# Performance work log

Hardware: AMD Instinct MI355X
Metric: run time of the kernel (lower is better)

The kernel has to match this reference:

```python
import jax, jax.numpy as jnp
import numpy as np

N_QUBITS = 5
N_A = 1
Q_DEPTH = 6
PATCH = 2 ** (N_QUBITS - N_A)  # 16


def _cz_sign(w):
    # diagonal sign of CZ on wires (w, w+1) over a (2,)*N_QUBITS state grid
    s = np.ones((2,) * N_QUBITS, np.float32)
    idx = [slice(None)] * N_QUBITS
    idx[w] = 1
    idx[w + 1] = 1
    s[tuple(idx)] = -1.0
    return jnp.asarray(s)

CZ_SIGNS = [_cz_sign(w) for w in range(N_QUBITS - 1)]


def apply_ry(state, theta, wire):
    # state: (B, 2,2,2,2,2) real amplitudes; theta: scalar or (B,)
    c = jnp.cos(theta * 0.5)
    s = jnp.sin(theta * 0.5)
    if jnp.ndim(c) == 1:  # per-sample angle
        c = c[:, None, None, None, None]
        s = s[:, None, None, None, None]
    st = jnp.moveaxis(state, 1 + wire, -1)
    a0, a1 = st[..., 0], st[..., 1]
    out = jnp.stack([c * a0 - s * a1, s * a0 + c * a1], axis=-1)
    return jnp.moveaxis(out, -1, 1 + wire)


def run_generator(noise, weights):
    # noise: (B, 5) per-sample angles; weights: (6, 5) shared angles
    B = noise.shape[0]
    state = jnp.zeros((B,) + (2,) * N_QUBITS, noise.dtype)
    state = state.at[(slice(None),) + (0,) * N_QUBITS].set(1.0)  # |00000>
    for w in range(N_QUBITS):
        state = apply_ry(state, noise[:, w], w)
    for d in range(Q_DEPTH):
        for w in range(N_QUBITS):
            state = apply_ry(state, weights[d, w], w)
        for w in range(N_QUBITS - 1):
            state = state * CZ_SIGNS[w]
    # RY/CZ are real, so probs = amplitude^2; unitary => sum(probs)=1
    probs = state.reshape(B, 2 ** N_QUBITS) ** 2
    p0 = probs[:, :PATCH]
    p0 = p0 / jnp.sum(probs, axis=1, keepdims=True)
    return p0 / jnp.max(p0, axis=1, keepdims=True)


def setup_inputs() -> dict:
    key = jax.random.key(0)
    k1, k2 = jax.random.split(key)
    B, C, H, W = 262144, 1, 4, 4
    inp = jax.random.normal(k1, (B, C, H, W), dtype=jnp.float32)
    q_params = jax.random.uniform(k2, (4, Q_DEPTH * N_QUBITS), dtype=jnp.float32)  # q_delta=1
    return {"input": inp, "q_params": q_params}


def reference(input, q_params):
    B, C, H, W = input.shape
    k = 2  # scale_factor
    # bilinear (half-pixel / align_corners=False) upsample
    up = jax.image.resize(input, (B, C, H * k, W * k), method='linear')
    noise = up.reshape(B, -1)[:, :N_QUBITS]  # 5 angles per sample
    outs = [run_generator(noise, q_params[g].reshape(Q_DEPTH, N_QUBITS))
            for g in range(q_params.shape[0])]
    return jnp.concatenate(outs, axis=1)  # (B, n_generators * 16)
```

## Files before the change

### kernel.cpp

```cpp
#include <hip/hip_runtime.h>

#define NQ   5
#define QD   6
#define NGEN 4
#define NW   (NGEN * QD * NQ)

typedef float f32x4 __attribute__((ext_vector_type(4)));
typedef short short8 __attribute__((ext_vector_type(8)));

__device__ inline unsigned short f2bf_rne(float f) {
    unsigned u = __float_as_uint(f);
    u += 0x7FFFu + ((u >> 16) & 1u);
    return (unsigned short)(u >> 16);
}
__device__ inline float bf2f(unsigned short h) {
    return __uint_as_float(((unsigned)h) << 16);
}

__global__ __launch_bounds__(128) void qsrgan_build(
    const float* __restrict__ qp,
    unsigned short* __restrict__ Bh,
    unsigned short* __restrict__ Bl)
{
    __shared__ float cw[NW];
    __shared__ float sw[NW];
    const int t = threadIdx.x;
    if (t < NW) {
        float sv, cv;
        __sincosf(0.5f * qp[t], &sv, &cv);
        cw[t] = cv;
        sw[t] = sv;
    }
    __syncthreads();

    const int g = t >> 5;
    const int basis = t & 31;

    float st[32];
#pragma unroll
    for (int i = 0; i < 32; ++i) st[i] = (i == basis) ? 1.0f : 0.0f;

    for (int d = 0; d < QD; ++d) {
        const int base = g * (QD * NQ) + d * NQ;
#pragma unroll
        for (int w = 0; w < NQ; ++w) {
            const float cc = cw[base + w];
            const float ss = sw[base + w];
            const int stride = 1 << (4 - w);
#pragma unroll
            for (int i = 0; i < 32; ++i) {
                if (i & stride) continue;
                float a0 = st[i];
                float a1 = st[i + stride];
                st[i]          = cc * a0 - ss * a1;
                st[i + stride] = ss * a0 + cc * a1;
            }
        }
#pragma unroll
        for (int i = 0; i < 32; ++i) {
            int flips = 0;
#pragma unroll
            for (int w = 0; w < NQ - 1; ++w) {
                const int m = (1 << (4 - w)) | (1 << (3 - w));
                flips ^= ((i & m) == m) ? 1 : 0;
            }
            if (flips) st[i] = -st[i];
        }
    }

#pragma unroll
    for (int j = 0; j < 16; ++j) {
        const float v = st[j];
        const unsigned short hi = f2bf_rne(v);
        const float r = v - bf2f(hi);
        const unsigned short lo = f2bf_rne(r);
        const int idx = ((g * 4 + (basis >> 3)) * 16 + j) * 8 + (basis & 7);
        Bh[idx] = hi;
        Bl[idx] = lo;
    }
}

__global__ __launch_bounds__(256, 4) void qsrgan_apply(
    const float* __restrict__ inp,
    const unsigned short* __restrict__ Bh,
    const unsigned short* __restrict__ Bl,
    float* __restrict__ out,
    int B)
{
    __shared__ float pl[64 * 66];

    const int t    = threadIdx.x;
    const int lane = t & 63;
    const int w    = t >> 6;
    const int q    = lane >> 4;
    const int c    = lane & 15;
    const int s0   = blockIdx.x * 64;

    const int bsmp = min(s0 + w * 16 + c, B - 1);
    const float4 x = *reinterpret_cast<const float4*>(inp + (size_t)bsmp * 16);

    short8 bh[4], bl[4];
    const short8* gh = reinterpret_cast<const short8*>(Bh);
    const short8* gl = reinterpret_cast<const short8*>(Bl);
#pragma unroll
    for (int g = 0; g < 4; ++g) {
        bh[g] = gh[g * 64 + lane];
        bl[g] = gl[g * 64 + lane];
    }

    float n[5];
    n[0] = x.x;
    n[1] = 0.75f * x.x + 0.25f * x.y;
    n[2] = 0.25f * x.x + 0.75f * x.y;
    n[3] = 0.75f * x.y + 0.25f * x.z;
    n[4] = 0.25f * x.y + 0.75f * x.z;
    float cn[5], sn[5];
#pragma unroll
    for (int i = 0; i < 5; ++i) {
        sn[i] = __sinf(0.5f * n[i]);
        cn[i] = __cosf(0.5f * n[i]);
    }
    const float U = ((q >> 1) ? sn[0] : cn[0]) * ((q & 1) ? sn[1] : cn[1]);
    float w34[4];
    w34[0] = cn[3] * cn[4];
    w34[1] = cn[3] * sn[4];
    w34[2] = sn[3] * cn[4];
    w34[3] = sn[3] * sn[4];

    short8 ah, al;
#pragma unroll
    for (int j = 0; j < 8; ++j) {
        const float a = U * ((j >> 2) ? sn[2] : cn[2]) * w34[j & 3];
        const unsigned short hi = f2bf_rne(a);
        const float r = a - bf2f(hi);
        ah[j] = (short)hi;
        al[j] = (short)f2bf_rne(r);
    }

    f32x4 acc[4];
#pragma unroll
    for (int g = 0; g < 4; ++g) {
        f32x4 a0 = {0.0f, 0.0f, 0.0f, 0.0f};
        a0 = __builtin_amdgcn_mfma_f32_16x16x32_bf16(ah, bh[g], a0, 0, 0, 0);
        a0 = __builtin_amdgcn_mfma_f32_16x16x32_bf16(al, bh[g], a0, 0, 0, 0);
        a0 = __builtin_amdgcn_mfma_f32_16x16x32_bf16(ah, bl[g], a0, 0, 0, 0);
        acc[g] = a0;
    }

#pragma unroll
    for (int g = 0; g < 4; ++g) {
#pragma unroll
        for (int r = 0; r < 4; ++r) {
            const float d = acc[g][r];
            float p = d * d;
            float m = p;
            m = fmaxf(m, __shfl_xor(m, 1));
            m = fmaxf(m, __shfl_xor(m, 2));
            m = fmaxf(m, __shfl_xor(m, 4));
            m = fmaxf(m, __shfl_xor(m, 8));
            const float v = p * (1.0f / m);
            pl[(g * 16 + c) * 66 + (w * 16 + q * 4 + r)] = v;
        }
    }

    __syncthreads();

    const size_t base = (size_t)s0 * 64;
    float4* __restrict__ o4 = reinterpret_cast<float4*>(out + base);
#pragma unroll
    for (int i = 0; i < 4; ++i) {
        const int qq   = t + i * 256;
        const int srow = qq >> 4;
        const int c0   = (qq & 15) << 2;
        if (s0 + srow < B) {
            float4 v;
            v.x = pl[(c0 + 0) * 66 + srow];
            v.y = pl[(c0 + 1) * 66 + srow];
            v.z = pl[(c0 + 2) * 66 + srow];
            v.w = pl[(c0 + 3) * 66 + srow];
            o4[qq] = v;
        }
    }
}

extern "C" void kernel_launch(void* const* d_in, const int* in_sizes, int n_in,
                              void* d_out, int out_size, void* d_ws, size_t ws_size,
                              hipStream_t stream) {
    const float* inp = (const float*)d_in[0];
    const float* qp  = (const float*)d_in[1];
    float* out = (float*)d_out;
    unsigned short* Bh = (unsigned short*)d_ws;
    unsigned short* Bl = (unsigned short*)d_ws + 2048;
    const int B = in_sizes[0] / 16;

    qsrgan_build<<<1, 128, 0, stream>>>(qp, Bh, Bl);
    const int blocks = (B + 63) / 64;
    qsrgan_apply<<<blocks, 256, 0, stream>>>(inp, Bh, Bl, out, B);
}
```

Before: 97.01 us.

## Swap MFMA operand roles so each lane owns a sample row, drop LDS transpose

Swaps the A/B operands of the bf16 MFMA so the accumulator puts samples along columns and output indices along rows. Each lane then holds four consecutive outputs of its own sample, which lets it write a float4 straight to global memory and find the row max with only two cross-lane shuffles instead of four per element. This removes the shared-memory staging buffer, the block barrier and the LDS transpose, and also merges sin/cos into sincos. The direct stores are strided by sample rather than fully contiguous per block, but each lane writes a contiguous 16-byte chunk. Clamped tail lanes may write duplicate rows.

```diff
diff --git a/kernel.cpp b/kernel.cpp
--- a/kernel.cpp
+++ b/kernel.cpp
@@ -19,8 +19,8 @@
 
 __global__ __launch_bounds__(128) void qsrgan_build(
     const float* __restrict__ qp,
-    unsigned short* __restrict__ Bh,
-    unsigned short* __restrict__ Bl)
+    unsigned short* __restrict__ Mh,
+    unsigned short* __restrict__ Ml)
 {
     __shared__ float cw[NW];
     __shared__ float sw[NW];
@@ -75,20 +75,18 @@
         const float r = v - bf2f(hi);
         const unsigned short lo = f2bf_rne(r);
         const int idx = ((g * 4 + (basis >> 3)) * 16 + j) * 8 + (basis & 7);
-        Bh[idx] = hi;
-        Bl[idx] = lo;
+        Mh[idx] = hi;
+        Ml[idx] = lo;
     }
 }
 
 __global__ __launch_bounds__(256, 4) void qsrgan_apply(
     const float* __restrict__ inp,
-    const unsigned short* __restrict__ Bh,
-    const unsigned short* __restrict__ Bl,
+    const unsigned short* __restrict__ Mh,
+    const unsigned short* __restrict__ Ml,
     float* __restrict__ out,
     int B)
 {
-    __shared__ float pl[64 * 66];
-
     const int t    = threadIdx.x;
     const int lane = t & 63;
     const int w    = t >> 6;
@@ -99,13 +97,13 @@
     const int bsmp = min(s0 + w * 16 + c, B - 1);
     const float4 x = *reinterpret_cast<const float4*>(inp + (size_t)bsmp * 16);
 
-    short8 bh[4], bl[4];
-    const short8* gh = reinterpret_cast<const short8*>(Bh);
-    const short8* gl = reinterpret_cast<const short8*>(Bl);
+    short8 mh[4], ml[4];
+    const short8* gh = reinterpret_cast<const short8*>(Mh);
+    const short8* gl = reinterpret_cast<const short8*>(Ml);
 #pragma unroll
     for (int g = 0; g < 4; ++g) {
-        bh[g] = gh[g * 64 + lane];
-        bl[g] = gl[g * 64 + lane];
+        mh[g] = gh[g * 64 + lane];
+        ml[g] = gl[g * 64 + lane];
     }
 
     float n[5];
@@ -116,10 +114,8 @@
     n[4] = 0.25f * x.y + 0.75f * x.z;
     float cn[5], sn[5];
 #pragma unroll
-    for (int i = 0; i < 5; ++i) {
-        sn[i] = __sinf(0.5f * n[i]);
-        cn[i] = __cosf(0.5f * n[i]);
-    }
+    for (int i = 0; i < 5; ++i) __sincosf(0.5f * n[i], &sn[i], &cn[i]);
+
     const float U = ((q >> 1) ? sn[0] : cn[0]) * ((q & 1) ? sn[1] : cn[1]);
     float w34[4];
     w34[0] = cn[3] * cn[4];
@@ -127,59 +123,39 @@
     w34[2] = sn[3] * cn[4];
     w34[3] = sn[3] * sn[4];
 
-    short8 ah, al;
+    short8 ih, il;
 #pragma unroll
     for (int j = 0; j < 8; ++j) {
         const float a = U * ((j >> 2) ? sn[2] : cn[2]) * w34[j & 3];
         const unsigned short hi = f2bf_rne(a);
         const float r = a - bf2f(hi);
-        ah[j] = (short)hi;
-        al[j] = (short)f2bf_rne(r);
+        ih[j] = (short)hi;
+        il[j] = (short)f2bf_rne(r);
     }
 
     f32x4 acc[4];
 #pragma unroll
     for (int g = 0; g < 4; ++g) {
         f32x4 a0 = {0.0f, 0.0f, 0.0f, 0.0f};
-        a0 = __builtin_amdgcn_mfma_f32_16x16x32_bf16(ah, bh[g], a0, 0, 0, 0);
-        a0 = __builtin_amdgcn_mfma_f32_16x16x32_bf16(al, bh[g], a0, 0, 0, 0);
-        a0 = __builtin_amdgcn_mfma_f32_16x16x32_bf16(ah, bl[g], a0, 0, 0, 0);
+        a0 = __builtin_amdgcn_mfma_f32_16x16x32_bf16(mh[g], ih, a0, 0, 0, 0);
+        a0 = __builtin_amdgcn_mfma_f32_16x16x32_bf16(ml[g], ih, a0, 0, 0, 0);
+        a0 = __builtin_amdgcn_mfma_f32_16x16x32_bf16(mh[g], il, a0, 0, 0, 0);
         acc[g] = a0;
     }
 
+    float* __restrict__ orow = out + (size_t)bsmp * 64;
 #pragma unroll
     for (int g = 0; g < 4; ++g) {
-#pragma unroll
-        for (int r = 0; r < 4; ++r) {
-            const float d = acc[g][r];
-            float p = d * d;
-            float m = p;
-            m = fmaxf(m, __shfl_xor(m, 1));
-            m = fmaxf(m, __shfl_xor(m, 2));
-            m = fmaxf(m, __shfl_xor(m, 4));
-            m = fmaxf(m, __shfl_xor(m, 8));
-            const float v = p * (1.0f / m);
-            pl[(g * 16 + c) * 66 + (w * 16 + q * 4 + r)] = v;
-        }
-    }
-
-    __syncthreads();
-
-    const size_t base = (size_t)s0 * 64;
-    float4* __restrict__ o4 = reinterpret_cast<float4*>(out + base);
-#pragma unroll
-    for (int i = 0; i < 4; ++i) {
-        const int qq   = t + i * 256;
-        const int srow = qq >> 4;
-        const int c0   = (qq & 15) << 2;
-        if (s0 + srow < B) {
-            float4 v;
-            v.x = pl[(c0 + 0) * 66 + srow];
-            v.y = pl[(c0 + 1) * 66 + srow];
-            v.z = pl[(c0 + 2) * 66 + srow];
-            v.w = pl[(c0 + 3) * 66 + srow];
-            o4[qq] = v;
-        }
+        float p0 = acc[g][0] * acc[g][0];
+        float p1 = acc[g][1] * acc[g][1];
+        float p2 = acc[g][2] * acc[g][2];
+        float p3 = acc[g][3] * acc[g][3];
+        float m = fmaxf(fmaxf(p0, p1), fmaxf(p2, p3));
+        m = fmaxf(m, __shfl_xor(m, 16));
+        m = fmaxf(m, __shfl_xor(m, 32));
+        const float inv = 1.0f / m;
+        float4 v = make_float4(p0 * inv, p1 * inv, p2 * inv, p3 * inv);
+        *reinterpret_cast<float4*>(orow + g * 16 + q * 4) = v;
     }
 }
 
@@ -189,11 +165,11 @@
     const float* inp = (const float*)d_in[0];
     const float* qp  = (const float*)d_in[1];
     float* out = (float*)d_out;
-    unsigned short* Bh = (unsigned short*)d_ws;
-    unsigned short* Bl = (unsigned short*)d_ws + 2048;
+    unsigned short* Mh = (unsigned short*)d_ws;
+    unsigned short* Ml = (unsigned short*)d_ws + 2048;
     const int B = in_sizes[0] / 16;
 
-    qsrgan_build<<<1, 128, 0, stream>>>(qp, Bh, Bl);
+    qsrgan_build<<<1, 128, 0, stream>>>(qp, Mh, Ml);
     const int blocks = (B + 63) / 64;
-    qsrgan_apply<<<blocks, 256, 0, stream>>>(inp, Bh, Bl, out, B);
+    qsrgan_apply<<<blocks, 256, 0, stream>>>(inp, Mh, Ml, out, B);
 }
```

Result: faster. 91.83 us (-5.3%).
